# Performance work log

Measured on AMD Instinct MI355X. Metric: run time of the kernel, lower is better.

## Reference

```python
import jax, jax.numpy as jnp
import numpy as np

EPS = 1e-5
H = 128
NA = 300000
NB = 600000
NBRS = 6

def _bn(x, gamma, beta):
    # BatchNorm1d in training mode: batch stats over dim 0, biased variance
    mu = jnp.mean(x, axis=0)
    var = jnp.mean((x - mu) ** 2, axis=0)
    return gamma * (x - mu) * jax.lax.rsqrt(var + EPS) + beta

def _lin(x, w, b):
    return x @ w.T + b

def setup_inputs() -> dict:
    key = jax.random.key(0)
    ks = jax.random.split(key, 20)
    s = 1.0 / np.sqrt(H)
    d = {
        'atom_layer_input': jax.random.normal(ks[0], (NA, H), jnp.float32),
        'bond_layer_input': jax.random.normal(ks[1], (NB, H), jnp.float32),
        'atom_adjacency_graph': jax.random.randint(ks[2], (NA, NBRS), 0, NA, jnp.int32),
        'atom_bond_adjacency_graph': jax.random.randint(ks[3], (NA, NBRS), 0, NB, jnp.int32),
        'bond_atom_adjacency_graph': jax.random.randint(ks[4], (NB, 2), 0, NA, jnp.int32),
    }
    names = ['U', 'V', 'A', 'B', 'C']
    for i, n in enumerate(names):
        d[n + '_w'] = jax.random.uniform(ks[5 + 2 * i], (H, H), jnp.float32, -s, s)
        d[n + '_b'] = jax.random.uniform(ks[6 + 2 * i], (H,), jnp.float32, -s, s)
    d['bn_bond_gamma'] = jnp.ones((H,), jnp.float32)
    d['bn_bond_beta'] = jnp.zeros((H,), jnp.float32)
    d['bn_atom_gamma'] = jnp.ones((H,), jnp.float32)
    d['bn_atom_beta'] = jnp.zeros((H,), jnp.float32)
    return d

def reference(atom_layer_input, bond_layer_input, atom_adjacency_graph,
              atom_bond_adjacency_graph, bond_atom_adjacency_graph,
              U_w, U_b, V_w, V_b, A_w, A_b, B_w, B_b, C_w, C_b,
              bn_bond_gamma, bn_bond_beta, bn_atom_gamma, bn_atom_beta):
    # --- edge (bond) update ---
    ex = atom_layer_input[bond_atom_adjacency_graph[:, 0]]  # [NB, H]
    ey = atom_layer_input[bond_atom_adjacency_graph[:, 1]]  # [NB, H]
    edge_syn = _lin(bond_layer_input, A_w, A_b) + _lin(ex, B_w, B_b) + _lin(ey, C_w, C_b)
    edge_gates = jax.nn.sigmoid(edge_syn)                    # [NB, H]
    edge_syn_bn = _bn(edge_syn, bn_bond_gamma, bn_bond_beta)
    bond_layer_output = jax.nn.relu(edge_syn_bn)             # residual overwritten in source
    # --- node (atom) update ---
    nbr_feats = atom_layer_input[atom_adjacency_graph]       # [NA, 6, H] gather
    nbr_V = jnp.einsum('nkh,oh->nko', nbr_feats, V_w) + V_b  # [NA, 6, H]
    nbr_gates = edge_gates[atom_bond_adjacency_graph]        # [NA, 6, H] gather
    msg = jnp.sum(nbr_gates * nbr_V, axis=1)                 # [NA, H]
    atom_syn = _lin(atom_layer_input, U_w, U_b) + msg
    atom_syn_bn = _bn(atom_syn, bn_atom_gamma, bn_atom_beta)
    atom_layer_output = jax.nn.relu(atom_syn_bn) + atom_layer_input  # residual (atom_feature_dim==0)
    return (atom_layer_output, bond_layer_output)
```

## Files before the change

### kernel.cpp

```cpp
#include <hip/hip_runtime.h>
#include <hip/hip_bf16.h>


#define H   128
#define NA  300000
#define NB  600000
#define EPS 1e-5f

#define NTILE_A (NA / 32)
#define NTILE_B (NB / 32)
#define GRID_A  1024
#define GRID_B  1024
#define EGRID   2048
#define BOUT_BLKS 512
#define MSG_BLKS  1536
#define FUSED_GRID (BOUT_BLKS + MSG_BLKS)
#define LDSW    136

typedef __attribute__((ext_vector_type(4)))  float  f32x4;
typedef __attribute__((ext_vector_type(16))) float  f32x16;
typedef __attribute__((ext_vector_type(8)))  __bf16 bfv8;
typedef __attribute__((ext_vector_type(4)))  unsigned short u16x4;
typedef __attribute__((ext_vector_type(8)))  unsigned short u16x8;

static __device__ __forceinline__ unsigned short f2bf(float f) {
    unsigned u = __float_as_uint(f);
    u = (u + 0x7fffu + ((u >> 16) & 1u)) >> 16;
    return (unsigned short)u;
}
static __device__ __forceinline__ float bf2f(unsigned short s) {
    return __uint_as_float(((unsigned)s) << 16);
}

static __device__ __forceinline__ void bar_lds() {
    asm volatile("s_waitcnt lgkmcnt(0)\n\ts_barrier" ::: "memory");
}

static __device__ __forceinline__ u16x8 pack2(f32x4 a, f32x4 b) {
    u16x8 w;
#pragma unroll
    for (int i = 0; i < 4; i++) { w[i] = f2bf(a[i]); w[i + 4] = f2bf(b[i]); }
    return w;
}

static __device__ __forceinline__ bfv8 load_frag(const float* __restrict__ p) {
    f32x4 a = *(const f32x4*)p, b = *(const f32x4*)(p + 4);
    bfv8 f;
#pragma unroll
    for (int i = 0; i < 4; i++) { f[i] = (__bf16)a[i]; f[i + 4] = (__bf16)b[i]; }
    return f;
}

__global__ __launch_bounds__(512, 4) void k_atom_gemm(
    const float* __restrict__ X,
    const float* __restrict__ Uw, const float* __restrict__ Vw,
    unsigned short* __restrict__ Uxo, unsigned short* __restrict__ Vxo,
    unsigned short* __restrict__ Xbf)
{
    __shared__ unsigned short xs[2][32 * LDSW];
    __shared__ unsigned short es[2][32 * LDSW];

    const int tid   = threadIdx.x;
    const int lane  = tid & 63;
    const int w     = tid >> 6;
    const int ng    = w & 3;
    const int pair  = w >> 2;
    const int l31   = lane & 31;
    const int khalf = lane >> 5;

    const int wrow_off = (ng * 32 + l31) * H + khalf * 8;
    const int cperm    = ng * 32 + khalf * 16;

    const float* W = pair ? Vw : Uw;
    bfv8 aw[8];
#pragma unroll
    for (int k = 0; k < 8; k++) aw[k] = load_frag(W + wrow_off + k * 16);

    const int srow = tid >> 4, sseg = tid & 15;
    const int g = tid >> 8, ft = tid & 255;
    const int frow = ft >> 3, fseg = ft & 7;
    unsigned short* O = g ? Vxo : Uxo;

    const int stride = gridDim.x;
    int t = blockIdx.x;

    f32x4 sl0, sl1;
    {
        const float* sp = X + (size_t)(t * 32 + srow) * H + sseg * 8;
        sl0 = *(const f32x4*)sp; sl1 = *(const f32x4*)(sp + 4);
        u16x8 pk = pack2(sl0, sl1);
        *(u16x8*)&xs[0][srow * LDSW + sseg * 8] = pk;
        *(u16x8*)(Xbf + (size_t)(t * 32 + srow) * H + sseg * 8) = pk;
    }
    __syncthreads();

    int p = 0;
#pragma unroll 1
    for (; t < NTILE_A; ) {
        const int tn = t + stride;
        const bool have = tn < NTILE_A;
        if (have) {
            const float* sp = X + (size_t)(tn * 32 + srow) * H + sseg * 8;
            sl0 = *(const f32x4*)sp; sl1 = *(const f32x4*)(sp + 4);
        }

        {
            const unsigned short* xrow = &xs[p][l31 * LDSW + khalf * 8];
            f32x16 acc;
#pragma unroll
            for (int i = 0; i < 16; i++) acc[i] = 0.0f;
#pragma unroll
            for (int k = 0; k < 8; k++) {
                bfv8 xf = *(const bfv8*)(xrow + k * 16);
                acc = __builtin_amdgcn_mfma_f32_32x32x16_bf16(aw[k], xf, acc, 0, 0, 0);
            }
            u16x8 o0, o1;
#pragma unroll
            for (int v = 0; v < 8; v++) { o0[v] = f2bf(acc[v]); o1[v] = f2bf(acc[v + 8]); }
            unsigned short* esw = &es[pair][l31 * LDSW + cperm];
            *(u16x8*)esw       = o0;
            *(u16x8*)(esw + 8) = o1;
        }
        bar_lds();

        {
            const unsigned short* esr = &es[g][frow * LDSW + fseg * 16];
            u16x8 e0 = *(const u16x8*)esr, e1 = *(const u16x8*)(esr + 8);
            const size_t fbase = (size_t)(t * 32 + frow) * H + fseg * 16;
            *(u16x8*)(O + fbase)     = e0;
            *(u16x8*)(O + fbase + 8) = e1;
        }
        if (have) {
            u16x8 pk = pack2(sl0, sl1);
            *(u16x8*)&xs[p ^ 1][srow * LDSW + sseg * 8] = pk;
            *(u16x8*)(Xbf + (size_t)(tn * 32 + srow) * H + sseg * 8) = pk;
        }
        bar_lds();
        p ^= 1;
        t = tn;
    }
}

__global__ __launch_bounds__(256, 2) void k_bond_gemm(
    const float* __restrict__ Xb, const unsigned short* __restrict__ Xbf,
    const float* __restrict__ Aw, const float* __restrict__ Bw,
    const float* __restrict__ Cw,
    const float* __restrict__ Ab, const float* __restrict__ Bb,
    const float* __restrict__ Cb,
    const int* __restrict__ g2,
    unsigned short* __restrict__ esyn,
    float* __restrict__ psum, float* __restrict__ psq)
{
    __shared__ unsigned short ts[3][32 * LDSW];
    __shared__ unsigned short es[32 * LDSW];
    __shared__ float bias_s[128];

    const int tid   = threadIdx.x;
    const int lane  = tid & 63;
    const int ng    = tid >> 6;
    const int l31   = lane & 31;
    const int khalf = lane >> 5;
    const int cperm = ng * 32 + khalf * 16;

    const int wro = (ng * 32 + l31) * H + khalf * 8;
    bfv8 awA[8], awB[8], awC[8];
#pragma unroll
    for (int k = 0; k < 8; k++) {
        awA[k] = load_frag(Aw + wro + k * 16);
        awB[k] = load_frag(Bw + wro + k * 16);
        awC[k] = load_frag(Cw + wro + k * 16);
    }

    if (tid < 128) {
        const int pcol = tid;
        const int grp = pcol >> 5, r = pcol & 31, kh = r >> 4, wi = r & 15;
        const int ct = grp * 32 + (wi >> 2) * 8 + kh * 4 + (wi & 3);
        bias_s[pcol] = Ab[ct] + Bb[ct] + Cb[ct];
    }

    const int srow = tid >> 3, sseg = tid & 7;

    float fs[16], fq[16];
#pragma unroll
    for (int i = 0; i < 16; i++) { fs[i] = 0.f; fq[i] = 0.f; }

    const int stride = gridDim.x;
    int t = blockIdx.x;

    f32x4 sxb[4];
    u16x8 re0, re1, ry0, ry1;
    int2 gg;

    {
        int2 g0 = *(const int2*)(g2 + 2 * (size_t)(t * 32 + srow));
        const float* sp = Xb + (size_t)(t * 32 + srow) * H + sseg * 16;
#pragma unroll
        for (int i = 0; i < 4; i++) sxb[i] = *(const f32x4*)(sp + 4 * i);
        const unsigned short* ep = Xbf + (size_t)g0.x * H + sseg * 16;
        re0 = *(const u16x8*)ep;  re1 = *(const u16x8*)(ep + 8);
        const unsigned short* yp = Xbf + (size_t)g0.y * H + sseg * 16;
        ry0 = *(const u16x8*)yp;  ry1 = *(const u16x8*)(yp + 8);
        const int tnx = t + stride;
        if (tnx < NTILE_B) gg = *(const int2*)(g2 + 2 * (size_t)(tnx * 32 + srow));
    }

#pragma unroll 1
    for (; t < NTILE_B; ) {
        const int tn = t + stride;
        const bool have = tn < NTILE_B;

        {
            const int off = srow * LDSW + sseg * 16;
            *(u16x8*)&ts[0][off]     = pack2(sxb[0], sxb[1]);
            *(u16x8*)&ts[0][off + 8] = pack2(sxb[2], sxb[3]);
            *(u16x8*)&ts[1][off]     = re0; *(u16x8*)&ts[1][off + 8] = re1;
            *(u16x8*)&ts[2][off]     = ry0; *(u16x8*)&ts[2][off + 8] = ry1;
        }
        bar_lds();

        if (have) {
            const float* sp = Xb + (size_t)(tn * 32 + srow) * H + sseg * 16;
#pragma unroll
            for (int i = 0; i < 4; i++) sxb[i] = *(const f32x4*)(sp + 4 * i);
            const unsigned short* ep = Xbf + (size_t)gg.x * H + sseg * 16;
            re0 = *(const u16x8*)ep;  re1 = *(const u16x8*)(ep + 8);
            const unsigned short* yp = Xbf + (size_t)gg.y * H + sseg * 16;
            ry0 = *(const u16x8*)yp;  ry1 = *(const u16x8*)(yp + 8);
            const int tnn = tn + stride;
            if (tnn < NTILE_B) gg = *(const int2*)(g2 + 2 * (size_t)(tnn * 32 + srow));
        }

        {
            const unsigned short* x0 = &ts[0][l31 * LDSW + khalf * 8];
            const unsigned short* x1 = &ts[1][l31 * LDSW + khalf * 8];
            const unsigned short* x2 = &ts[2][l31 * LDSW + khalf * 8];
            f32x16 acc;
#pragma unroll
            for (int i = 0; i < 16; i++) acc[i] = 0.0f;
#pragma unroll
            for (int k = 0; k < 8; k++)
                acc = __builtin_amdgcn_mfma_f32_32x32x16_bf16(awA[k], *(const bfv8*)(x0 + k * 16), acc, 0, 0, 0);
#pragma unroll
            for (int k = 0; k < 8; k++)
                acc = __builtin_amdgcn_mfma_f32_32x32x16_bf16(awB[k], *(const bfv8*)(x1 + k * 16), acc, 0, 0, 0);
#pragma unroll
            for (int k = 0; k < 8; k++)
                acc = __builtin_amdgcn_mfma_f32_32x32x16_bf16(awC[k], *(const bfv8*)(x2 + k * 16), acc, 0, 0, 0);
            u16x8 o0, o1;
#pragma unroll
            for (int v = 0; v < 8; v++) { o0[v] = f2bf(acc[v]); o1[v] = f2bf(acc[v + 8]); }
            unsigned short* esw = &es[l31 * LDSW + cperm];
            *(u16x8*)esw       = o0;
            *(u16x8*)(esw + 8) = o1;
        }
        bar_lds();

        {
            const unsigned short* esr = &es[srow * LDSW + sseg * 16];
            u16x8 e0 = *(const u16x8*)esr, e1 = *(const u16x8*)(esr + 8);
            const float* bp = bias_s + sseg * 16;
            u16x8 w0, w1;
#pragma unroll
            for (int i = 0; i < 8; i++) {
                float v = bf2f(e0[i]) + bp[i];
                w0[i] = f2bf(v); fs[i] += v; fq[i] += v * v;
            }
#pragma unroll
            for (int i = 0; i < 8; i++) {
                float v = bf2f(e1[i]) + bp[8 + i];
                w1[i] = f2bf(v); fs[8 + i] += v; fq[8 + i] += v * v;
            }
            unsigned short* op = esyn + (size_t)(t * 32 + srow) * H + sseg * 16;
            *(u16x8*)op       = w0;
            *(u16x8*)(op + 8) = w1;
        }
        t = tn;
    }

    float* red = (float*)es;
    for (int i = 0; i < 16; i++) {
        __syncthreads();
        red[tid] = fs[i]; red[256 + tid] = fq[i];
        __syncthreads();
        if (tid < 8) {
            float S = 0.f, Q = 0.f;
            for (int r = 0; r < 32; r++) { S += red[r * 8 + tid]; Q += red[256 + r * 8 + tid]; }
            psum[(size_t)blockIdx.x * H + tid * 16 + i] = S;
            psq [(size_t)blockIdx.x * H + tid * 16 + i] = Q;
        }
    }
}

__global__ void k_bn_stats(const float* __restrict__ psum, const float* __restrict__ psq,
                           int nblk, float invN,
                           const float* __restrict__ gamma, const float* __restrict__ beta,
                           float* __restrict__ scale, float* __restrict__ shift)
{
    __shared__ float ls[256], lq[256];
    const int c = blockIdx.x;
    float s = 0.f, q = 0.f;
    for (int i = threadIdx.x; i < nblk; i += 256) {
        s += psum[(size_t)i * H + c];
        q += psq [(size_t)i * H + c];
    }
    ls[threadIdx.x] = s; lq[threadIdx.x] = q;
    __syncthreads();
    for (int off = 128; off > 0; off >>= 1) {
        if ((int)threadIdx.x < off) {
            ls[threadIdx.x] += ls[threadIdx.x + off];
            lq[threadIdx.x] += lq[threadIdx.x + off];
        }
        __syncthreads();
    }
    if (threadIdx.x == 0) {
        const int r = c & 31, kh = r >> 4, wi = r & 15;
        const int ct = (c & ~31) + (wi >> 2) * 8 + kh * 4 + (wi & 3);
        float mean = ls[0] * invN;
        float var  = lq[0] * invN - mean * mean;
        float sc   = gamma[ct] * rsqrtf(var + EPS);
        scale[c] = sc;
        shift[c] = beta[ct] - mean * sc;
    }
}

__global__ __launch_bounds__(256) void k_bout_amsg(
    const unsigned short* __restrict__ esyn,
    float* __restrict__ out_bond,
    const float* __restrict__ scale, const float* __restrict__ shift,
    const unsigned short* __restrict__ Ux,
    const unsigned short* __restrict__ Vx,
    const int* __restrict__ adj,
    const int* __restrict__ abadj,
    const float* __restrict__ Ub, const float* __restrict__ Vb,
    unsigned short* __restrict__ syn_a,
    float* __restrict__ psum, float* __restrict__ psq)
{
    __shared__ float ls[256][8], lq[256][8];

    if (blockIdx.x < BOUT_BLKS) {
        const size_t total  = (size_t)NB * (H / 8);
        const size_t stride = (size_t)BOUT_BLKS * 256;
        const int c0 = (threadIdx.x & 15) * 8;
        const f32x4 sc0 = *(const f32x4*)(scale + c0), sc1 = *(const f32x4*)(scale + c0 + 4);
        const f32x4 sh0 = *(const f32x4*)(shift + c0), sh1 = *(const f32x4*)(shift + c0 + 4);
        const int tc0 = (c0 & ~31) + (((c0 >> 2) & 3) * 8) + ((c0 >> 4) & 1) * 4;
        const int tc1 = tc0 + 8;
        for (size_t i = (size_t)blockIdx.x * 256 + threadIdx.x; i < total; i += stride) {
            u16x8 v = ((const u16x8*)esyn)[i];
            const size_t row = i >> 4;
            f32x4 o0, o1;
#pragma unroll
            for (int j = 0; j < 4; j++) {
                o0[j] = fmaxf(bf2f(v[j])     * sc0[j] + sh0[j], 0.0f);
                o1[j] = fmaxf(bf2f(v[j + 4]) * sc1[j] + sh1[j], 0.0f);
            }
            float* yp = out_bond + row * H;
            *(f32x4*)(yp + tc0) = o0;
            *(f32x4*)(yp + tc1) = o1;
        }
        return;
    }

    const int bid = blockIdx.x - BOUT_BLKS;
    const int cg = threadIdx.x & 15;
    const int rh = threadIdx.x >> 4;
    const int c0 = cg * 8;
    const int tc0 = (c0 & ~31) + (((c0 >> 2) & 3) * 8) + ((c0 >> 4) & 1) * 4;
    const f32x4 ub0 = *(const f32x4*)(Ub + tc0), ub1 = *(const f32x4*)(Ub + tc0 + 8);
    const f32x4 vb0 = *(const f32x4*)(Vb + tc0), vb1 = *(const f32x4*)(Vb + tc0 + 8);

    float s[8], q[8];
#pragma unroll
    for (int j = 0; j < 8; j++) { s[j] = 0.f; q[j] = 0.f; }

    const int rstride = MSG_BLKS * 16;
    int r = bid * 16 + rh;

    int2 A[3], Bv[3];
    if (r < NA) {
#pragma unroll
        for (int p = 0; p < 3; p++) {
            A[p]  = *(const int2*)(adj   + (size_t)r * 6 + 2 * p);
            Bv[p] = *(const int2*)(abadj + (size_t)r * 6 + 2 * p);
        }
    }

#pragma unroll 1
    for (; r < NA; ) {
        const int rn = r + rstride;

        const int ai[6] = {A[0].x, A[0].y, A[1].x, A[1].y, A[2].x, A[2].y};
        const int bi[6] = {Bv[0].x, Bv[0].y, Bv[1].x, Bv[1].y, Bv[2].x, Bv[2].y};

        u16x8 uv = *(const u16x8*)(Ux + (size_t)r * H + c0);

        if (rn < NA) {
#pragma unroll
            for (int p = 0; p < 3; p++) {
                A[p]  = *(const int2*)(adj   + (size_t)rn * 6 + 2 * p);
                Bv[p] = *(const int2*)(abadj + (size_t)rn * 6 + 2 * p);
            }
        }

        float v[8];
#pragma unroll
        for (int j = 0; j < 4; j++) {
            v[j]     = bf2f(uv[j])     + ub0[j];
            v[j + 4] = bf2f(uv[j + 4]) + ub1[j];
        }
#pragma unroll
        for (int k = 0; k < 6; k++) {
            u16x8 vx = *(const u16x8*)(Vx   + (size_t)ai[k] * H + c0);
            u16x8 es = *(const u16x8*)(esyn + (size_t)bi[k] * H + c0);
#pragma unroll
            for (int j = 0; j < 4; j++) {
                float g0 = 1.0f / (1.0f + __expf(-bf2f(es[j])));
                float g1 = 1.0f / (1.0f + __expf(-bf2f(es[j + 4])));
                v[j]     += g0 * (bf2f(vx[j])     + vb0[j]);
                v[j + 4] += g1 * (bf2f(vx[j + 4]) + vb1[j]);
            }
        }
        u16x8 ov;
#pragma unroll
        for (int j = 0; j < 8; j++) ov[j] = f2bf(v[j]);
        *(u16x8*)(syn_a + (size_t)r * H + c0) = ov;
#pragma unroll
        for (int j = 0; j < 8; j++) { s[j] += v[j]; q[j] += v[j] * v[j]; }

        r = rn;
    }

#pragma unroll
    for (int j = 0; j < 8; j++) { ls[threadIdx.x][j] = s[j]; lq[threadIdx.x][j] = q[j]; }
    __syncthreads();
    if (threadIdx.x < 128) {
        const int c = threadIdx.x, g = c >> 3, j = c & 7;
        float S = 0.f, Q = 0.f;
        for (int rg = 0; rg < 16; rg++) { S += ls[rg * 16 + g][j]; Q += lq[rg * 16 + g][j]; }
        psum[(size_t)bid * H + c] = S;
        psq [(size_t)bid * H + c] = Q;
    }
}

__global__ __launch_bounds__(256) void k_atom_out(const unsigned short* __restrict__ syn,
                                                  const unsigned short* __restrict__ xbf,
                                                  float* __restrict__ y,
                                                  const float* __restrict__ scale,
                                                  const float* __restrict__ shift)
{
    const size_t total  = (size_t)NA * (H / 8);
    const size_t stride = (size_t)gridDim.x * 256;
    const int c0 = (threadIdx.x & 15) * 8;
    const f32x4 sc0 = *(const f32x4*)(scale + c0), sc1 = *(const f32x4*)(scale + c0 + 4);
    const f32x4 sh0 = *(const f32x4*)(shift + c0), sh1 = *(const f32x4*)(shift + c0 + 4);
    const int tc0 = (c0 & ~31) + (((c0 >> 2) & 3) * 8) + ((c0 >> 4) & 1) * 4;
    const int tc1 = tc0 + 8;
    for (size_t i = (size_t)blockIdx.x * 256 + threadIdx.x; i < total; i += stride) {
        u16x8 v = ((const u16x8*)syn)[i];
        const size_t row = i >> 4;
        const unsigned short* xp = xbf + row * H;
        u16x4 x0 = *(const u16x4*)(xp + tc0);
        u16x4 x1 = *(const u16x4*)(xp + tc1);
        f32x4 o0, o1;
#pragma unroll
        for (int j = 0; j < 4; j++) {
            o0[j] = fmaxf(bf2f(v[j])     * sc0[j] + sh0[j], 0.0f) + bf2f(x0[j]);
            o1[j] = fmaxf(bf2f(v[j + 4]) * sc1[j] + sh1[j], 0.0f) + bf2f(x1[j]);
        }
        float* yp = y + row * H;
        *(f32x4*)(yp + tc0) = o0;
        *(f32x4*)(yp + tc1) = o1;
    }
}

extern "C" void kernel_launch(void* const* d_in, const int* in_sizes, int n_in,
                              void* d_out, int out_size, void* d_ws, size_t ws_size,
                              hipStream_t stream)
{
    const float* X     = (const float*)d_in[0];
    const float* Xb    = (const float*)d_in[1];
    const int*   adj   = (const int*)d_in[2];
    const int*   abadj = (const int*)d_in[3];
    const int*   g2    = (const int*)d_in[4];
    const float* Uw = (const float*)d_in[5],  *Ub = (const float*)d_in[6];
    const float* Vw = (const float*)d_in[7],  *Vb = (const float*)d_in[8];
    const float* Aw = (const float*)d_in[9],  *Ab = (const float*)d_in[10];
    const float* Bw = (const float*)d_in[11], *Bb = (const float*)d_in[12];
    const float* Cw = (const float*)d_in[13], *Cb = (const float*)d_in[14];
    const float* gb = (const float*)d_in[15], *bb = (const float*)d_in[16];
    const float* ga = (const float*)d_in[17], *ba = (const float*)d_in[18];

    float* out_atom = (float*)d_out;
    float* out_bond = out_atom + (size_t)NA * H;

    char* ws = (char*)d_ws;
    size_t o = 0;
    unsigned short* Ux    = (unsigned short*)(ws + o); o += (size_t)NA * H * 2;
    unsigned short* Vx    = (unsigned short*)(ws + o); o += (size_t)NA * H * 2;
    unsigned short* Xbf   = (unsigned short*)(ws + o); o += (size_t)NA * H * 2;
    unsigned short* esyn  = (unsigned short*)(ws + o); o += (size_t)NB * H * 2;
    unsigned short* syn_a = (unsigned short*)(ws + o); o += (size_t)NA * H * 2;
    float* psum_b = (float*)(ws + o);  o += (size_t)EGRID * H * 4;
    float* psq_b  = (float*)(ws + o);  o += (size_t)EGRID * H * 4;
    float* psum_a = (float*)(ws + o);  o += (size_t)EGRID * H * 4;
    float* psq_a  = (float*)(ws + o);  o += (size_t)EGRID * H * 4;
    float* scale_b = (float*)(ws + o); o += 512;
    float* shift_b = (float*)(ws + o); o += 512;
    float* scale_a = (float*)(ws + o); o += 512;
    float* shift_a = (float*)(ws + o); o += 512;
    (void)o; (void)ws_size; (void)in_sizes; (void)n_in; (void)out_size;

    k_atom_gemm<<<GRID_A, 512, 0, stream>>>(X, Uw, Vw, Ux, Vx, Xbf);
    k_bond_gemm<<<GRID_B, 256, 0, stream>>>(Xb, Xbf, Aw, Bw, Cw, Ab, Bb, Cb, g2,
                                            esyn, psum_b, psq_b);
    k_bn_stats<<<H, 256, 0, stream>>>(psum_b, psq_b, GRID_B, 1.0f / NB, gb, bb, scale_b, shift_b);
    k_bout_amsg<<<FUSED_GRID, 256, 0, stream>>>(esyn, out_bond, scale_b, shift_b,
                                                Ux, Vx, adj, abadj, Ub, Vb,
                                                syn_a, psum_a, psq_a);
    k_bn_stats<<<H, 256, 0, stream>>>(psum_a, psq_a, MSG_BLKS, 1.0f / NA, ga, ba, scale_a, shift_a);
    k_atom_out<<<EGRID, 256, 0, stream>>>(syn_a, Xbf, out_atom, scale_a, shift_a);
}
```

Before: 536.9 us.

## Deepen bond GEMM gather prefetch to two tiles ahead, raise occupancy

The bond GEMM loop now handles two tiles (A and B) per iteration. Each tile's gathered atom rows are prefetched two strides ahead in separate register sets, giving the random gathers more time to land before use. It also cuts the grid from 1024 to 768 blocks and raises the launch-bounds occupancy hint from 2 to 3 blocks per SIMD. The extra prefetch registers raise register pressure, which can conflict with the higher occupancy target and cause spills. The partial per-block statistics are sized by the new grid.

```diff
diff --git a/kernel.cpp b/kernel.cpp
--- a/kernel.cpp
+++ b/kernel.cpp
@@ -10,7 +10,7 @@
 #define NTILE_A (NA / 32)
 #define NTILE_B (NB / 32)
 #define GRID_A  1024
-#define GRID_B  1024
+#define GRID_B  768
 #define EGRID   2048
 #define BOUT_BLKS 512
 #define MSG_BLKS  1536
@@ -141,7 +141,7 @@
     }
 }
 
-__global__ __launch_bounds__(256, 2) void k_bond_gemm(
+__global__ __launch_bounds__(256, 3) void k_bond_gemm(
     const float* __restrict__ Xb, const unsigned short* __restrict__ Xbf,
     const float* __restrict__ Aw, const float* __restrict__ Bw,
     const float* __restrict__ Cw,
@@ -185,49 +185,55 @@
     for (int i = 0; i < 16; i++) { fs[i] = 0.f; fq[i] = 0.f; }
 
     const int stride = gridDim.x;
-    int t = blockIdx.x;
+    const int s2 = 2 * stride;
 
     f32x4 sxb[4];
-    u16x8 re0, re1, ry0, ry1;
-    int2 gg;
+    u16x8 reA0, reA1, ryA0, ryA1;
+    u16x8 reB0, reB1, ryB0, ryB1;
+    int2 ggA, ggB;
+
+    int tA = blockIdx.x;
+    int tB = tA + stride;
+
+#define LOAD_XB(T)                                                             \
+    {                                                                          \
+        const float* sp_ = Xb + (size_t)((T) * 32 + srow) * H + sseg * 16;     \
+        _Pragma("unroll") for (int i_ = 0; i_ < 4; i_++)                       \
+            sxb[i_] = *(const f32x4*)(sp_ + 4 * i_);                           \
+    }
+#define GATHER(G, E0, E1, Y0, Y1)                                              \
+    {                                                                          \
+        const unsigned short* ep_ = Xbf + (size_t)(G).x * H + sseg * 16;       \
+        E0 = *(const u16x8*)ep_;  E1 = *(const u16x8*)(ep_ + 8);               \
+        const unsigned short* yp_ = Xbf + (size_t)(G).y * H + sseg * 16;       \
+        Y0 = *(const u16x8*)yp_;  Y1 = *(const u16x8*)(yp_ + 8);               \
+    }
+#define G2ROW(T) (*(const int2*)(g2 + 2 * (size_t)((T) * 32 + srow)))
 
     {
-        int2 g0 = *(const int2*)(g2 + 2 * (size_t)(t * 32 + srow));
-        const float* sp = Xb + (size_t)(t * 32 + srow) * H + sseg * 16;
-#pragma unroll
-        for (int i = 0; i < 4; i++) sxb[i] = *(const f32x4*)(sp + 4 * i);
-        const unsigned short* ep = Xbf + (size_t)g0.x * H + sseg * 16;
-        re0 = *(const u16x8*)ep;  re1 = *(const u16x8*)(ep + 8);
-        const unsigned short* yp = Xbf + (size_t)g0.y * H + sseg * 16;
-        ry0 = *(const u16x8*)yp;  ry1 = *(const u16x8*)(yp + 8);
-        const int tnx = t + stride;
-        if (tnx < NTILE_B) gg = *(const int2*)(g2 + 2 * (size_t)(tnx * 32 + srow));
+        int2 g0 = G2ROW(tA);
+        LOAD_XB(tA);
+        GATHER(g0, reA0, reA1, ryA0, ryA1);
+        if (tB < NTILE_B) { int2 g1 = G2ROW(tB); GATHER(g1, reB0, reB1, ryB0, ryB1); }
+        if (tA + s2 < NTILE_B) ggA = G2ROW(tA + s2);
+        if (tB + s2 < NTILE_B) ggB = G2ROW(tB + s2);
     }
 
 #pragma unroll 1
-    for (; t < NTILE_B; ) {
-        const int tn = t + stride;
-        const bool have = tn < NTILE_B;
-
+    for (; tA < NTILE_B; ) {
         {
             const int off = srow * LDSW + sseg * 16;
             *(u16x8*)&ts[0][off]     = pack2(sxb[0], sxb[1]);
             *(u16x8*)&ts[0][off + 8] = pack2(sxb[2], sxb[3]);
-            *(u16x8*)&ts[1][off]     = re0; *(u16x8*)&ts[1][off + 8] = re1;
-            *(u16x8*)&ts[2][off]     = ry0; *(u16x8*)&ts[2][off + 8] = ry1;
+            *(u16x8*)&ts[1][off]     = reA0; *(u16x8*)&ts[1][off + 8] = reA1;
+            *(u16x8*)&ts[2][off]     = ryA0; *(u16x8*)&ts[2][off + 8] = ryA1;
         }
         bar_lds();
 
-        if (have) {
-            const float* sp = Xb + (size_t)(tn * 32 + srow) * H + sseg * 16;
-#pragma unroll
-            for (int i = 0; i < 4; i++) sxb[i] = *(const f32x4*)(sp + 4 * i);
-            const unsigned short* ep = Xbf + (size_t)gg.x * H + sseg * 16;
-            re0 = *(const u16x8*)ep;  re1 = *(const u16x8*)(ep + 8);
-            const unsigned short* yp = Xbf + (size_t)gg.y * H + sseg * 16;
-            ry0 = *(const u16x8*)yp;  ry1 = *(const u16x8*)(yp + 8);
-            const int tnn = tn + stride;
-            if (tnn < NTILE_B) gg = *(const int2*)(g2 + 2 * (size_t)(tnn * 32 + srow));
+        if (tB < NTILE_B) LOAD_XB(tB);
+        if (tA + s2 < NTILE_B) {
+            GATHER(ggA, reA0, reA1, ryA0, ryA1);
+            if (tA + 2 * s2 < NTILE_B) ggA = G2ROW(tA + 2 * s2);
         }
 
         {
@@ -270,12 +276,79 @@
                 float v = bf2f(e1[i]) + bp[8 + i];
                 w1[i] = f2bf(v); fs[8 + i] += v; fq[8 + i] += v * v;
             }
-            unsigned short* op = esyn + (size_t)(t * 32 + srow) * H + sseg * 16;
+            unsigned short* op = esyn + (size_t)(tA * 32 + srow) * H + sseg * 16;
             *(u16x8*)op       = w0;
             *(u16x8*)(op + 8) = w1;
         }
-        t = tn;
-    }
+
+        if (tB < NTILE_B) {
+            bar_lds();
+            {
+                const int off = srow * LDSW + sseg * 16;
+                *(u16x8*)&ts[0][off]     = pack2(sxb[0], sxb[1]);
+                *(u16x8*)&ts[0][off + 8] = pack2(sxb[2], sxb[3]);
+                *(u16x8*)&ts[1][off]     = reB0; *(u16x8*)&ts[1][off + 8] = reB1;
+                *(u16x8*)&ts[2][off]     = ryB0; *(u16x8*)&ts[2][off + 8] = ryB1;
+            }
+            bar_lds();
+
+            if (tA + s2 < NTILE_B) LOAD_XB(tA + s2);
+            if (tB + s2 < NTILE_B) {
+                GATHER(ggB, reB0, reB1, ryB0, ryB1);
+                if (tB + 2 * s2 < NTILE_B) ggB = G2ROW(tB + 2 * s2);
+            }
+
+            {
+                const unsigned short* x0 = &ts[0][l31 * LDSW + khalf * 8];
+                const unsigned short* x1 = &ts[1][l31 * LDSW + khalf * 8];
+                const unsigned short* x2 = &ts[2][l31 * LDSW + khalf * 8];
+                f32x16 acc;
+#pragma unroll
+                for (int i = 0; i < 16; i++) acc[i] = 0.0f;
+#pragma unroll
+                for (int k = 0; k < 8; k++)
+                    acc = __builtin_amdgcn_mfma_f32_32x32x16_bf16(awA[k], *(const bfv8*)(x0 + k * 16), acc, 0, 0, 0);
+#pragma unroll
+                for (int k = 0; k < 8; k++)
+                    acc = __builtin_amdgcn_mfma_f32_32x32x16_bf16(awB[k], *(const bfv8*)(x1 + k * 16), acc, 0, 0, 0);
+#pragma unroll
+                for (int k = 0; k < 8; k++)
+                    acc = __builtin_amdgcn_mfma_f32_32x32x16_bf16(awC[k], *(const bfv8*)(x2 + k * 16), acc, 0, 0, 0);
+                u16x8 o0, o1;
+#pragma unroll
+                for (int v = 0; v < 8; v++) { o0[v] = f2bf(acc[v]); o1[v] = f2bf(acc[v + 8]); }
+                unsigned short* esw = &es[l31 * LDSW + cperm];
+                *(u16x8*)esw       = o0;
+                *(u16x8*)(esw + 8) = o1;
+            }
+            bar_lds();
+
+            {
+                const unsigned short* esr = &es[srow * LDSW + sseg * 16];
+                u16x8 e0 = *(const u16x8*)esr, e1 = *(const u16x8*)(esr + 8);
+                const float* bp = bias_s + sseg * 16;
+                u16x8 w0, w1;
+#pragma unroll
+                for (int i = 0; i < 8; i++) {
+                    float v = bf2f(e0[i]) + bp[i];
+                    w0[i] = f2bf(v); fs[i] += v; fq[i] += v * v;
+                }
+#pragma unroll
+                for (int i = 0; i < 8; i++) {
+                    float v = bf2f(e1[i]) + bp[8 + i];
+                    w1[i] = f2bf(v); fs[8 + i] += v; fq[8 + i] += v * v;
+                }
+                unsigned short* op = esyn + (size_t)(tB * 32 + srow) * H + sseg * 16;
+                *(u16x8*)op       = w0;
+                *(u16x8*)(op + 8) = w1;
+            }
+            bar_lds();
+        }
+        tA += s2; tB += s2;
+    }
+#undef LOAD_XB
+#undef GATHER
+#undef G2ROW
 
     float* red = (float*)es;
     for (int i = 0; i < 16; i++) {
```

Measured after the change: 734.3 us. 1.37x slower.
